# Kernel optimization log

Hardware: AMD Instinct MI355X
Metric: run time of the kernel (lower is better)

Reference implementation:

```python
import jax, jax.numpy as jnp
import numpy as np
from jax import lax

LIDAR_MAX_X = 30.0
LIDAR_MAX_Y = 30.0


def bilinear_sample(value, grid):
    """value: (bs,C,H,W); grid: (bs,nq,np,2) in [-1,1] -> (bs,C,nq,np)."""
    bs, C, H, W = value.shape
    _, nq, npts, _ = grid.shape
    gx = (grid[..., 0] + 1.0) / 2.0 * (W - 1)
    gy = (grid[..., 1] + 1.0) / 2.0 * (H - 1)
    # torch .long() truncates; in-bounds coords are non-negative so trunc == floor
    x0 = jnp.clip(gx.astype(jnp.int32), 0, W - 2)
    y0 = jnp.clip(gy.astype(jnp.int32), 0, H - 2)
    x1 = x0 + 1
    y1 = y0 + 1
    wx = jnp.clip(gx - x0.astype(gx.dtype), 0.0, 1.0).reshape(bs, 1, -1)
    wy = jnp.clip(gy - y0.astype(gy.dtype), 0.0, 1.0).reshape(bs, 1, -1)
    x0f = x0.reshape(bs, -1); x1f = x1.reshape(bs, -1)
    y0f = y0.reshape(bs, -1); y1f = y1.reshape(bs, -1)
    vflat = value.reshape(bs, C, H * W)
    gather = jax.vmap(lambda v, i: v[:, i])  # (C,HW),(N,) -> (C,N)
    v00 = gather(vflat, y0f * W + x0f)
    v01 = gather(vflat, y0f * W + x1f)
    v10 = gather(vflat, y1f * W + x0f)
    v11 = gather(vflat, y1f * W + x1f)
    sampled = (v00 * (1 - wx) * (1 - wy) + v01 * wx * (1 - wy)
               + v10 * (1 - wx) * wy + v11 * wx * wy)
    sampled = sampled.reshape(bs, C, nq, npts)
    gx0, gy0 = grid[..., 0], grid[..., 1]
    in_bounds = ((gx0 >= -1) & (gx0 <= 1) & (gy0 >= -1) & (gy0 <= 1))
    return sampled * in_bounds[:, None].astype(sampled.dtype)


def setup_inputs() -> dict:
    key = jax.random.key(0)
    ks = jax.random.split(key, 8)
    bs, nq, npts = 8, 2048, 8
    C_in, H, W = 64, 200, 200
    D = 256
    queries = jax.random.normal(ks[0], (bs, nq, D), dtype=jnp.float32)
    # lidar-frame waypoints, mostly in-bounds
    traj_points = jax.random.uniform(ks[1], (bs, nq, npts, 2), jnp.float32, -30.0, 30.0)
    bev_feature = jax.random.normal(ks[2], (bs, C_in, H, W), dtype=jnp.float32)
    attn_w = jax.random.normal(ks[3], (npts, D), dtype=jnp.float32) * 0.05
    attn_b = jnp.zeros((npts,), jnp.float32)
    out_w = jax.random.normal(ks[4], (D, D), dtype=jnp.float32) * (1.0 / np.sqrt(D))
    out_b = jnp.zeros((D,), jnp.float32)
    conv_w = jax.random.normal(ks[5], (D, C_in, 3, 3), dtype=jnp.float32) * 0.05
    conv_b = jnp.zeros((D,), jnp.float32)
    return {"queries": queries, "traj_points": traj_points, "bev_feature": bev_feature,
            "attn_w": attn_w, "attn_b": attn_b, "out_w": out_w, "out_b": out_b,
            "conv_w": conv_w, "conv_b": conv_b}


def reference(queries, traj_points, bev_feature, attn_w, attn_b, out_w, out_b, conv_w, conv_b):
    # normalize trajectory and swap (x,y) -> (y,x)
    norm = traj_points / jnp.array([LIDAR_MAX_Y, LIDAR_MAX_X], dtype=traj_points.dtype)
    grid = norm[..., ::-1]  # (bs,nq,np,2)
    # per-point attention weights
    attw = jax.nn.softmax(jnp.einsum('bqd,pd->bqp', queries, attn_w) + attn_b, axis=-1)
    # value projection: Conv3x3 + ReLU
    value = lax.conv_general_dilated(bev_feature, conv_w, (1, 1), ((1, 1), (1, 1)),
                                     dimension_numbers=('NCHW', 'OIHW', 'NCHW'))
    value = jax.nn.relu(value + conv_b[None, :, None, None])
    sampled = lax.stop_gradient(bilinear_sample(value, grid))  # (bs,C,nq,np)
    out = jnp.einsum('bcqp,bqp->bqc', sampled, attw)  # weighted sum over points
    out = jnp.einsum('bqc,dc->bqd', out, out_w) + out_b
    return out + queries  # dropout is identity in eval mode
```

## Files before the change

### kernel.cpp

```cpp
#include <hip/hip_runtime.h>

typedef unsigned short u16;
typedef _Float16 f16x8 __attribute__((ext_vector_type(8)));
typedef _Float16 f16x2 __attribute__((ext_vector_type(2)));
typedef float f32x4 __attribute__((ext_vector_type(4)));

__device__ __forceinline__ u16 f2h(float f){
  _Float16 h = (_Float16)f;
  return __builtin_bit_cast(u16, h);
}

__device__ __forceinline__ void load_lds16(const void* g, void* l){
  __builtin_amdgcn_global_load_lds((const __attribute__((address_space(1))) void*)g,
                                   (__attribute__((address_space(3))) void*)l,
                                   16, 0, 0);
}

__global__ __launch_bounds__(256) void kv9_halo(u16* __restrict__ bevT)
{
  const int i = blockIdx.x * 256 + threadIdx.x;
  if (i >= 8*804*8) return;
  const int b = i / (804*8);
  const int rem = i - b*(804*8);
  const int p = rem >> 3, c = rem & 7;
  int h, w;
  if (p < 202)      { h = 0;        w = p; }
  else if (p < 404) { h = 201;      w = p - 202; }
  else if (p < 604) { h = p - 403;  w = 0; }
  else              { h = p - 603;  w = 201; }
  const uint4 z = {0u,0u,0u,0u};
  *(uint4*)&bevT[(((size_t)b*202 + h)*202 + w)*64 + (c << 3)] = z;
}

__global__ __launch_bounds__(256) void kv9_transpose(const float* __restrict__ bev,
                                                     u16* __restrict__ bevT)
{
  __shared__ float t[64][65];
  const int tid = threadIdx.x;
  const int bid = blockIdx.x;
  const int wc = bid & 3;
  const int h  = (bid >> 2) % 200;
  const int b  = bid / 800;
  const int w0 = wc << 6;

  const int wl = (tid & 15) << 2;
  const int cb = tid >> 4;
  if (w0 + wl < 200){
    #pragma unroll
    for (int r = 0; r < 4; ++r){
      const int c = cb + (r << 4);
      const float4 v = *(const float4*)&bev[(((size_t)b*64 + c)*200 + h)*200 + (w0 + wl)];
      t[c][wl] = v.x; t[c][wl+1] = v.y; t[c][wl+2] = v.z; t[c][wl+3] = v.w;
    }
  }
  __syncthreads();
  const int c0 = (tid & 7) << 3;
  #pragma unroll
  for (int j = 0; j < 2; ++j){
    const int wl2 = (tid >> 3) + (j << 5);
    if (w0 + wl2 < 200){
      unsigned r0 = (unsigned)f2h(t[c0+0][wl2]) | ((unsigned)f2h(t[c0+1][wl2]) << 16);
      unsigned r1 = (unsigned)f2h(t[c0+2][wl2]) | ((unsigned)f2h(t[c0+3][wl2]) << 16);
      unsigned r2 = (unsigned)f2h(t[c0+4][wl2]) | ((unsigned)f2h(t[c0+5][wl2]) << 16);
      unsigned r3 = (unsigned)f2h(t[c0+6][wl2]) | ((unsigned)f2h(t[c0+7][wl2]) << 16);
      uint4 o = {r0, r1, r2, r3};
      *(uint4*)&bevT[(((size_t)b*202 + h + 1)*202 + (w0 + wl2 + 1))*64 + c0] = o;
    }
  }
}

__global__ __launch_bounds__(256) void kv9_prep(const float* __restrict__ conv_w,
                                                const float* __restrict__ out_w,
                                                u16* __restrict__ Wr,
                                                u16* __restrict__ owb)
{
  const int i = blockIdx.x * 256 + threadIdx.x;
  if (i < 9*256*64){
    const int t9 = i / (256*64);
    const int rem = i - t9*(256*64);
    const int d = rem >> 6, c = rem & 63;
    Wr[i] = f2h(conv_w[(size_t)(d*64 + c)*9 + t9]);
  } else {
    const int j = i - 9*256*64;
    if (j < 65536) owb[j] = f2h(out_w[j]);
  }
}

__global__ __launch_bounds__(256) void kv9_attw(const float* __restrict__ q,
                                                const float* __restrict__ aw,
                                                const float* __restrict__ ab,
                                                float* __restrict__ attw)
{
  const int lane = threadIdx.x & 63;
  const int bq = blockIdx.x * 4 + (threadIdx.x >> 6);
  const float4 qv = *(const float4*)&q[(size_t)bq*256 + (lane << 2)];
  float lg[8];
  #pragma unroll
  for (int p = 0; p < 8; ++p){
    const float4 wv = *(const float4*)&aw[p*256 + (lane << 2)];
    float d = qv.x*wv.x + qv.y*wv.y + qv.z*wv.z + qv.w*wv.w;
    #pragma unroll
    for (int off = 32; off > 0; off >>= 1) d += __shfl_xor(d, off);
    lg[p] = d + ab[p];
  }
  float mx = lg[0];
  #pragma unroll
  for (int p = 1; p < 8; ++p) mx = fmaxf(mx, lg[p]);
  float sum = 0.f;
  #pragma unroll
  for (int p = 0; p < 8; ++p){ lg[p] = expf(lg[p] - mx); sum += lg[p]; }
  const float inv = 1.f / sum;
  if (lane == 0){
    float4 o0 = {lg[0]*inv, lg[1]*inv, lg[2]*inv, lg[3]*inv};
    float4 o1 = {lg[4]*inv, lg[5]*inv, lg[6]*inv, lg[7]*inv};
    *(float4*)&attw[(size_t)bq*8]     = o0;
    *(float4*)&attw[(size_t)bq*8 + 4] = o1;
  }
}

__global__ __launch_bounds__(256) void kv9_conv(const u16* __restrict__ bevT,
                                                const u16* __restrict__ Wr,
                                                const float* __restrict__ conv_b,
                                                u16* __restrict__ value)
{
  __shared__ __align__(16) u16 lds[16384];
  const int tid  = threadIdx.x;
  const int bid  = (int)(blockIdx.x & 7) * 625 + (int)(blockIdx.x >> 3);
  const int n0   = (bid & 1) << 7;
  const int m0   = (bid >> 1) << 7;
  const int lane = tid & 63;
  const int wv   = tid >> 6;
  const int wm   = (wv >> 1) << 6;
  const int wn   = (wv & 1) << 6;
  const int c0   = (((tid & 7) ^ ((tid >> 3) & 7)) << 3);

  int baseA[4], baseB[4];
  #pragma unroll
  for (int i = 0; i < 4; ++i){
    const int m = m0 + (i << 5) + (tid >> 3);
    const int b = m / 40000;
    const int pix = m - b * 40000;
    const int h = pix / 200;
    const int w = pix - h * 200;
    baseA[i] = ((b*202 + h)*202 + w)*64 + c0;
    baseB[i] = (n0 + (i << 5) + (tid >> 3))*64 + c0;
  }

  const f32x4 z = {0.f, 0.f, 0.f, 0.f};
  f32x4 acc[4][4];
  #pragma unroll
  for (int mf = 0; mf < 4; ++mf)
    #pragma unroll
    for (int nf = 0; nf < 4; ++nf)
      acc[mf][nf] = z;

  const int swz = lane & 7;
  for (int t9 = 0; t9 < 9; ++t9){
    const int ky = t9 / 3;
    const int offA = (ky*202 + (t9 - ky*3))*64;
    const u16* wsrc = Wr + t9*16384;
    #pragma unroll
    for (int i = 0; i < 4; ++i){
      load_lds16(bevT + baseA[i] + offA, lds + (i << 11) + (wv << 9));
      load_lds16(wsrc + baseB[i],        lds + 8192 + (i << 11) + (wv << 9));
    }
    __syncthreads();

    f16x8 a_frag[2][4], b_frag[2][4];
    #pragma unroll
    for (int kh = 0; kh < 2; ++kh){
      const int c16 = (((kh << 2) + (lane >> 4)) ^ swz) << 3;
      #pragma unroll
      for (int f = 0; f < 4; ++f){
        a_frag[kh][f] = *(const f16x8*)&lds[(wm + (f << 4) + (lane & 15))*64 + c16];
        b_frag[kh][f] = *(const f16x8*)&lds[8192 + (wn + (f << 4) + (lane & 15))*64 + c16];
      }
    }
    #pragma unroll
    for (int kh = 0; kh < 2; ++kh)
      #pragma unroll
      for (int mf = 0; mf < 4; ++mf)
        #pragma unroll
        for (int nf = 0; nf < 4; ++nf)
          acc[mf][nf] = __builtin_amdgcn_mfma_f32_16x16x32_f16(a_frag[kh][mf], b_frag[kh][nf], acc[mf][nf], 0, 0, 0);
    __syncthreads();
  }

  #pragma unroll
  for (int nf = 0; nf < 4; ++nf){
    const int col = wn + (nf << 4) + (lane & 15);
    const float bias = conv_b[n0 + col];
    #pragma unroll
    for (int mf = 0; mf < 4; ++mf)
      #pragma unroll
      for (int rr = 0; rr < 4; ++rr){
        const int row = wm + (mf << 4) + ((lane >> 4) << 2) + rr;
        lds[row*128 + col] = f2h(fmaxf(acc[mf][nf][rr] + bias, 0.f));
      }
  }
  __syncthreads();
  #pragma unroll
  for (int it = 0; it < 8; ++it){
    const int idx = (it << 8) + tid;
    const int row = idx >> 4;
    const int ce  = (idx & 15) << 3;
    const f32x4 v = *(const f32x4*)&lds[row*128 + ce];
    *(f32x4*)&value[(size_t)(m0 + row)*256 + n0 + ce] = v;
  }
}

__global__ __launch_bounds__(256) void kv9_sample(const float* __restrict__ traj,
                                                  const float* __restrict__ attw,
                                                  const u16* __restrict__ value,
                                                  u16* __restrict__ sbh)
{
  __shared__ int   pixs[2][32];
  __shared__ float wgts[2][32];
  const int tid  = threadIdx.x;
  const int half = tid >> 7;
  const int t    = tid & 127;
  const int q    = (blockIdx.x << 1) + half;

  if (t < 8){
    const int p = t;
    const float ty = traj[((size_t)q*8 + p)*2 + 0];
    const float tx = traj[((size_t)q*8 + p)*2 + 1];
    float aw = attw[q*8 + p];
    const float gxn = tx / 30.f;
    const float gyn = ty / 30.f;
    if (!(gxn >= -1.f && gxn <= 1.f && gyn >= -1.f && gyn <= 1.f)) aw = 0.f;
    const float gx = (gxn + 1.f) * 0.5f * 199.f;
    const float gy = (gyn + 1.f) * 0.5f * 199.f;
    int x0 = (int)gx; x0 = min(max(x0, 0), 198);
    int y0 = (int)gy; y0 = min(max(y0, 0), 198);
    const float wx = fminf(fmaxf(gx - (float)x0, 0.f), 1.f);
    const float wy = fminf(fmaxf(gy - (float)y0, 0.f), 1.f);
    const int base = y0*200 + x0;
    pixs[half][p*4+0] = base;       wgts[half][p*4+0] = aw*(1.f-wx)*(1.f-wy);
    pixs[half][p*4+1] = base+1;     wgts[half][p*4+1] = aw*wx*(1.f-wy);
    pixs[half][p*4+2] = base+200;   wgts[half][p*4+2] = aw*(1.f-wx)*wy;
    pixs[half][p*4+3] = base+201;   wgts[half][p*4+3] = aw*wx*wy;
  }
  __syncthreads();
  const size_t vbase = (size_t)(q >> 11) * 40000;
  float a0 = 0.f, a1 = 0.f;
  #pragma unroll
  for (int i = 0; i < 32; ++i){
    const float w = wgts[half][i];
    const f16x2 pv = *(const f16x2*)&value[((vbase + pixs[half][i]) << 8) + (t << 1)];
    a0 = fmaf(w, (float)pv.x, a0);
    a1 = fmaf(w, (float)pv.y, a1);
  }
  const unsigned o = (unsigned)f2h(a0) | ((unsigned)f2h(a1) << 16);
  *(unsigned*)&sbh[((size_t)q << 8) + (t << 1)] = o;
}

__global__ __launch_bounds__(256) void kv9_outgemm(const u16* __restrict__ sbh,
                                                   const u16* __restrict__ owb,
                                                   const float* __restrict__ out_b,
                                                   const float* __restrict__ queries,
                                                   float* __restrict__ outp)
{
  __shared__ __align__(16) u16 lds[16384];
  const int tid  = threadIdx.x;
  const int bid  = blockIdx.x;
  const int n0   = (bid & 1) << 7;
  const int m0   = (bid >> 1) << 7;
  const int lane = tid & 63;
  const int wv   = tid >> 6;
  const int wm   = (wv >> 1) << 6;
  const int wn   = (wv & 1) << 6;
  const int c0   = (tid & 7) << 3;

  int baseA[4], baseB[4];
  #pragma unroll
  for (int i = 0; i < 4; ++i){
    baseA[i] = (m0 + (i << 5) + (tid >> 3))*256 + c0;
    baseB[i] = (n0 + (i << 5) + (tid >> 3))*256 + c0;
  }
  const f32x4 z = {0.f, 0.f, 0.f, 0.f};
  f32x4 acc[4][4];
  #pragma unroll
  for (int mf = 0; mf < 4; ++mf)
    #pragma unroll
    for (int nf = 0; nf < 4; ++nf)
      acc[mf][nf] = z;

  for (int kk = 0; kk < 4; ++kk){
    #pragma unroll
    for (int i = 0; i < 4; ++i){
      load_lds16(sbh + baseA[i] + (kk << 6), lds + (i << 11) + (wv << 9));
      load_lds16(owb + baseB[i] + (kk << 6), lds + 8192 + (i << 11) + (wv << 9));
    }
    __syncthreads();

    f16x8 a_frag[2][4], b_frag[2][4];
    #pragma unroll
    for (int kh = 0; kh < 2; ++kh){
      const int kq = (kh << 5) + ((lane >> 4) << 3);
      #pragma unroll
      for (int f = 0; f < 4; ++f){
        a_frag[kh][f] = *(const f16x8*)&lds[(wm + (f << 4) + (lane & 15))*64 + kq];
        b_frag[kh][f] = *(const f16x8*)&lds[8192 + (wn + (f << 4) + (lane & 15))*64 + kq];
      }
    }
    #pragma unroll
    for (int kh = 0; kh < 2; ++kh)
      #pragma unroll
      for (int mf = 0; mf < 4; ++mf)
        #pragma unroll
        for (int nf = 0; nf < 4; ++nf)
          acc[mf][nf] = __builtin_amdgcn_mfma_f32_16x16x32_f16(a_frag[kh][mf], b_frag[kh][nf], acc[mf][nf], 0, 0, 0);
    __syncthreads();
  }

  #pragma unroll
  for (int nf = 0; nf < 4; ++nf){
    const int col = wn + (nf << 4) + (lane & 15);
    const float ob = out_b[n0 + col];
    #pragma unroll
    for (int mf = 0; mf < 4; ++mf)
      #pragma unroll
      for (int rr = 0; rr < 4; ++rr){
        const int row = wm + (mf << 4) + ((lane >> 4) << 2) + rr;
        const size_t off = (size_t)(m0 + row)*256 + n0 + col;
        outp[off] = acc[mf][nf][rr] + ob + queries[off];
      }
  }
}

extern "C" void kernel_launch(void* const* d_in, const int* in_sizes, int n_in,
                              void* d_out, int out_size, void* d_ws, size_t ws_size,
                              hipStream_t stream)
{
  const float* queries = (const float*)d_in[0];
  const float* traj    = (const float*)d_in[1];
  const float* bev     = (const float*)d_in[2];
  const float* attn_w  = (const float*)d_in[3];
  const float* attn_b  = (const float*)d_in[4];
  const float* out_w   = (const float*)d_in[5];
  const float* out_b   = (const float*)d_in[6];
  const float* conv_w  = (const float*)d_in[7];
  const float* conv_b  = (const float*)d_in[8];
  float* outp = (float*)d_out;
  char* ws = (char*)d_ws;

  u16*   bevT  = (u16*)  (ws + 0);
  u16*   value = (u16*)  (ws + 41783296);
  u16*   Wr    = (u16*)  (ws + 205623296);
  u16*   owb   = (u16*)  (ws + 205918208);
  float* attw  = (float*)(ws + 206049280);
  u16*   sbh   = (u16*)  (ws + 206573568);

  kv9_halo     <<<201,  256, 0, stream>>>(bevT);
  kv9_transpose<<<6400, 256, 0, stream>>>(bev, bevT);
  kv9_prep     <<<832,  256, 0, stream>>>(conv_w, out_w, Wr, owb);
  kv9_attw     <<<4096, 256, 0, stream>>>(queries, attn_w, attn_b, attw);
  kv9_conv     <<<5000, 256, 0, stream>>>(bevT, Wr, conv_b, value);
  kv9_sample   <<<8192, 256, 0, stream>>>(traj, attw, value, sbh);
  kv9_outgemm  <<<256,  256, 0, stream>>>(sbh, owb, out_b, queries, outp);
}
```

Before: 206.0 us.

## Double-buffer conv LDS tiles to prefetch next tap during MFMA compute

The implicit-GEMM conv kernel now uses two LDS buffers, issuing the async global-to-LDS loads for the next 3x3 tap before computing the current one. It waits with explicit vmcnt counts and raw barriers instead of __syncthreads, and raises wave priority around the MFMA block. The aim is to hide global load latency behind matrix math. The cost is doubled LDS (64KB per block), which may lower occupancy, and hand-tuned waitcnt logic that must match the issued load count.

```diff
diff --git a/kernel.cpp b/kernel.cpp
--- a/kernel.cpp
+++ b/kernel.cpp
@@ -16,7 +16,7 @@
                                    16, 0, 0);
 }
 
-__global__ __launch_bounds__(256) void kv9_halo(u16* __restrict__ bevT)
+__global__ __launch_bounds__(256) void kv10_halo(u16* __restrict__ bevT)
 {
   const int i = blockIdx.x * 256 + threadIdx.x;
   if (i >= 8*804*8) return;
@@ -32,8 +32,8 @@
   *(uint4*)&bevT[(((size_t)b*202 + h)*202 + w)*64 + (c << 3)] = z;
 }
 
-__global__ __launch_bounds__(256) void kv9_transpose(const float* __restrict__ bev,
-                                                     u16* __restrict__ bevT)
+__global__ __launch_bounds__(256) void kv10_transpose(const float* __restrict__ bev,
+                                                      u16* __restrict__ bevT)
 {
   __shared__ float t[64][65];
   const int tid = threadIdx.x;
@@ -69,10 +69,10 @@
   }
 }
 
-__global__ __launch_bounds__(256) void kv9_prep(const float* __restrict__ conv_w,
-                                                const float* __restrict__ out_w,
-                                                u16* __restrict__ Wr,
-                                                u16* __restrict__ owb)
+__global__ __launch_bounds__(256) void kv10_prep(const float* __restrict__ conv_w,
+                                                 const float* __restrict__ out_w,
+                                                 u16* __restrict__ Wr,
+                                                 u16* __restrict__ owb)
 {
   const int i = blockIdx.x * 256 + threadIdx.x;
   if (i < 9*256*64){
@@ -86,10 +86,10 @@
   }
 }
 
-__global__ __launch_bounds__(256) void kv9_attw(const float* __restrict__ q,
-                                                const float* __restrict__ aw,
-                                                const float* __restrict__ ab,
-                                                float* __restrict__ attw)
+__global__ __launch_bounds__(256) void kv10_attw(const float* __restrict__ q,
+                                                 const float* __restrict__ aw,
+                                                 const float* __restrict__ ab,
+                                                 float* __restrict__ attw)
 {
   const int lane = threadIdx.x & 63;
   const int bq = blockIdx.x * 4 + (threadIdx.x >> 6);
@@ -118,12 +118,12 @@
   }
 }
 
-__global__ __launch_bounds__(256) void kv9_conv(const u16* __restrict__ bevT,
-                                                const u16* __restrict__ Wr,
-                                                const float* __restrict__ conv_b,
-                                                u16* __restrict__ value)
-{
-  __shared__ __align__(16) u16 lds[16384];
+__global__ __launch_bounds__(256) void kv10_conv(const u16* __restrict__ bevT,
+                                                 const u16* __restrict__ Wr,
+                                                 const float* __restrict__ conv_b,
+                                                 u16* __restrict__ value)
+{
+  __shared__ __align__(16) u16 lds[32768];
   const int tid  = threadIdx.x;
   const int bid  = (int)(blockIdx.x & 7) * 625 + (int)(blockIdx.x >> 3);
   const int n0   = (bid & 1) << 7;
@@ -154,28 +154,42 @@
     for (int nf = 0; nf < 4; ++nf)
       acc[mf][nf] = z;
 
+#define STAGE(buf, t9) do{                                                 \
+    const int ky_ = (t9)/3;                                                \
+    const int offA_ = (ky_*202 + ((t9) - ky_*3))*64;                       \
+    const u16* ws_ = Wr + (t9)*16384;                                      \
+    _Pragma("unroll")                                                      \
+    for (int i_ = 0; i_ < 4; ++i_){                                        \
+      load_lds16(bevT + baseA[i_] + offA_,                                 \
+                 lds + (buf)*16384 + (i_ << 11) + (wv << 9));              \
+      load_lds16(ws_ + baseB[i_],                                          \
+                 lds + (buf)*16384 + 8192 + (i_ << 11) + (wv << 9));       \
+    } }while(0)
+
+  STAGE(0, 0);
+
   const int swz = lane & 7;
+  #pragma unroll
   for (int t9 = 0; t9 < 9; ++t9){
-    const int ky = t9 / 3;
-    const int offA = (ky*202 + (t9 - ky*3))*64;
-    const u16* wsrc = Wr + t9*16384;
-    #pragma unroll
-    for (int i = 0; i < 4; ++i){
-      load_lds16(bevT + baseA[i] + offA, lds + (i << 11) + (wv << 9));
-      load_lds16(wsrc + baseB[i],        lds + 8192 + (i << 11) + (wv << 9));
-    }
-    __syncthreads();
-
+    const int cur = t9 & 1;
+    if (t9 < 8) STAGE(cur ^ 1, t9 + 1);
+
+    if (t9 < 8) asm volatile("s_waitcnt vmcnt(8)" ::: "memory");
+    else        asm volatile("s_waitcnt vmcnt(0)" ::: "memory");
+    __builtin_amdgcn_s_barrier();
+
+    const u16* Lb = lds + cur*16384;
     f16x8 a_frag[2][4], b_frag[2][4];
     #pragma unroll
     for (int kh = 0; kh < 2; ++kh){
       const int c16 = (((kh << 2) + (lane >> 4)) ^ swz) << 3;
       #pragma unroll
       for (int f = 0; f < 4; ++f){
-        a_frag[kh][f] = *(const f16x8*)&lds[(wm + (f << 4) + (lane & 15))*64 + c16];
-        b_frag[kh][f] = *(const f16x8*)&lds[8192 + (wn + (f << 4) + (lane & 15))*64 + c16];
+        a_frag[kh][f] = *(const f16x8*)&Lb[(wm + (f << 4) + (lane & 15))*64 + c16];
+        b_frag[kh][f] = *(const f16x8*)&Lb[8192 + (wn + (f << 4) + (lane & 15))*64 + c16];
       }
     }
+    __builtin_amdgcn_s_setprio(1);
     #pragma unroll
     for (int kh = 0; kh < 2; ++kh)
       #pragma unroll
@@ -183,8 +197,12 @@
         #pragma unroll
         for (int nf = 0; nf < 4; ++nf)
           acc[mf][nf] = __builtin_amdgcn_mfma_f32_16x16x32_f16(a_frag[kh][mf], b_frag[kh][nf], acc[mf][nf], 0, 0, 0);
-    __syncthreads();
-  }
+    __builtin_amdgcn_s_setprio(0);
+
+    asm volatile("s_waitcnt lgkmcnt(0)" ::: "memory");
+    __builtin_amdgcn_s_barrier();
+  }
+#undef STAGE
 
   #pragma unroll
   for (int nf = 0; nf < 4; ++nf){
@@ -209,10 +227,10 @@
   }
 }
 
-__global__ __launch_bounds__(256) void kv9_sample(const float* __restrict__ traj,
-                                                  const float* __restrict__ attw,
-                                                  const u16* __restrict__ value,
-                                                  u16* __restrict__ sbh)
+__global__ __launch_bounds__(256) void kv10_sample(const float* __restrict__ traj,
+                                                   const float* __restrict__ attw,
+                                                   const u16* __restrict__ value,
+                                                   u16* __restrict__ sbh)
 {
   __shared__ int   pixs[2][32];
   __shared__ float wgts[2][32];
@@ -255,11 +273,11 @@
   *(unsigned*)&sbh[((size_t)q << 8) + (t << 1)] = o;
 }
 
-__global__ __launch_bounds__(256) void kv9_outgemm(const u16* __restrict__ sbh,
-                                                   const u16* __restrict__ owb,
-                                                   const float* __restrict__ out_b,
-                                                   const float* __restrict__ queries,
-                                                   float* __restrict__ outp)
+__global__ __launch_bounds__(256) void kv10_outgemm(const u16* __restrict__ sbh,
+                                                    const u16* __restrict__ owb,
+                                                    const float* __restrict__ out_b,
+                                                    const float* __restrict__ queries,
+                                                    float* __restrict__ outp)
 {
   __shared__ __align__(16) u16 lds[16384];
   const int tid  = threadIdx.x;
@@ -352,11 +370,11 @@
   float* attw  = (float*)(ws + 206049280);
   u16*   sbh   = (u16*)  (ws + 206573568);
 
-  kv9_halo     <<<201,  256, 0, stream>>>(bevT);
-  kv9_transpose<<<6400, 256, 0, stream>>>(bev, bevT);
-  kv9_prep     <<<832,  256, 0, stream>>>(conv_w, out_w, Wr, owb);
-  kv9_attw     <<<4096, 256, 0, stream>>>(queries, attn_w, attn_b, attw);
-  kv9_conv     <<<5000, 256, 0, stream>>>(bevT, Wr, conv_b, value);
-  kv9_sample   <<<8192, 256, 0, stream>>>(traj, attw, value, sbh);
-  kv9_outgemm  <<<256,  256, 0, stream>>>(sbh, owb, out_b, queries, outp);
-}
+  kv10_halo     <<<201,  256, 0, stream>>>(bevT);
+  kv10_transpose<<<6400, 256, 0, stream>>>(bev, bevT);
+  kv10_prep     <<<832,  256, 0, stream>>>(conv_w, out_w, Wr, owb);
+  kv10_attw     <<<4096, 256, 0, stream>>>(queries, attn_w, attn_b, attw);
+  kv10_conv     <<<5000, 256, 0, stream>>>(bevT, Wr, conv_b, value);
+  kv10_sample   <<<8192, 256, 0, stream>>>(traj, attw, value, sbh);
+  kv10_outgemm  <<<256,  256, 0, stream>>>(sbh, owb, out_b, queries, outp);
+}
```

Result: no change. 202.4 us (-1.8%).

## Double-buffer conv A tiles, load B fragments to registers, remap sample blocks

Applied to the files above, without the earlier changes.

The conv kernel now double-buffers the im2col A tiles in LDS, prefetching the next tap while MFMAs run on the current one. Weight B fragments are loaded straight from global memory into registers (ping-pong bE/bO) instead of being staged through LDS. It adds manual waitcnt/barriers, setprio, and a launch-bounds occupancy hint of 2. The sample kernel's block-to-query mapping is interleaved across batches so that concurrent blocks spread over different batch slices of the value tensor. The added register pressure from B fragments and the manual vmcnt counting risk spills or ordering bugs.

```diff
diff --git a/kernel.cpp b/kernel.cpp
--- a/kernel.cpp
+++ b/kernel.cpp
@@ -16,7 +16,7 @@
                                    16, 0, 0);
 }
 
-__global__ __launch_bounds__(256) void kv9_halo(u16* __restrict__ bevT)
+__global__ __launch_bounds__(256) void kv12_halo(u16* __restrict__ bevT)
 {
   const int i = blockIdx.x * 256 + threadIdx.x;
   if (i >= 8*804*8) return;
@@ -32,8 +32,8 @@
   *(uint4*)&bevT[(((size_t)b*202 + h)*202 + w)*64 + (c << 3)] = z;
 }
 
-__global__ __launch_bounds__(256) void kv9_transpose(const float* __restrict__ bev,
-                                                     u16* __restrict__ bevT)
+__global__ __launch_bounds__(256) void kv12_transpose(const float* __restrict__ bev,
+                                                      u16* __restrict__ bevT)
 {
   __shared__ float t[64][65];
   const int tid = threadIdx.x;
@@ -69,10 +69,10 @@
   }
 }
 
-__global__ __launch_bounds__(256) void kv9_prep(const float* __restrict__ conv_w,
-                                                const float* __restrict__ out_w,
-                                                u16* __restrict__ Wr,
-                                                u16* __restrict__ owb)
+__global__ __launch_bounds__(256) void kv12_prep(const float* __restrict__ conv_w,
+                                                 const float* __restrict__ out_w,
+                                                 u16* __restrict__ Wr,
+                                                 u16* __restrict__ owb)
 {
   const int i = blockIdx.x * 256 + threadIdx.x;
   if (i < 9*256*64){
@@ -86,10 +86,10 @@
   }
 }
 
-__global__ __launch_bounds__(256) void kv9_attw(const float* __restrict__ q,
-                                                const float* __restrict__ aw,
-                                                const float* __restrict__ ab,
-                                                float* __restrict__ attw)
+__global__ __launch_bounds__(256) void kv12_attw(const float* __restrict__ q,
+                                                 const float* __restrict__ aw,
+                                                 const float* __restrict__ ab,
+                                                 float* __restrict__ attw)
 {
   const int lane = threadIdx.x & 63;
   const int bq = blockIdx.x * 4 + (threadIdx.x >> 6);
@@ -118,10 +118,10 @@
   }
 }
 
-__global__ __launch_bounds__(256) void kv9_conv(const u16* __restrict__ bevT,
-                                                const u16* __restrict__ Wr,
-                                                const float* __restrict__ conv_b,
-                                                u16* __restrict__ value)
+__global__ __launch_bounds__(256, 2) void kv12_conv(const u16* __restrict__ bevT,
+                                                    const u16* __restrict__ Wr,
+                                                    const float* __restrict__ conv_b,
+                                                    u16* __restrict__ value)
 {
   __shared__ __align__(16) u16 lds[16384];
   const int tid  = threadIdx.x;
@@ -134,7 +134,7 @@
   const int wn   = (wv & 1) << 6;
   const int c0   = (((tid & 7) ^ ((tid >> 3) & 7)) << 3);
 
-  int baseA[4], baseB[4];
+  int baseA[4];
   #pragma unroll
   for (int i = 0; i < 4; ++i){
     const int m = m0 + (i << 5) + (tid >> 3);
@@ -143,8 +143,12 @@
     const int h = pix / 200;
     const int w = pix - h * 200;
     baseA[i] = ((b*202 + h)*202 + w)*64 + c0;
-    baseB[i] = (n0 + (i << 5) + (tid >> 3))*64 + c0;
-  }
+  }
+  const int ko = (lane >> 4) << 3;
+  int rowB[4];
+  #pragma unroll
+  for (int f = 0; f < 4; ++f)
+    rowB[f] = ((n0 + wn + (f << 4) + (lane & 15)) << 6) + ko;
 
   const f32x4 z = {0.f, 0.f, 0.f, 0.f};
   f32x4 acc[4][4];
@@ -154,37 +158,79 @@
     for (int nf = 0; nf < 4; ++nf)
       acc[mf][nf] = z;
 
+  f16x8 bE[2][4], bO[2][4];
+
+#define STAGE_A(buf, t9) do{                                               \
+    const int ky_ = (t9)/3;                                                \
+    const int offA_ = (ky_*202 + ((t9) - ky_*3))*64;                       \
+    _Pragma("unroll")                                                      \
+    for (int i_ = 0; i_ < 4; ++i_)                                         \
+      load_lds16(bevT + baseA[i_] + offA_,                                 \
+                 lds + (buf)*8192 + (i_ << 11) + (wv << 9));               \
+  }while(0)
+
+#define LOADB(dst, t9) do{                                                 \
+    const u16* ws_ = Wr + (t9)*16384;                                      \
+    _Pragma("unroll")                                                      \
+    for (int f_ = 0; f_ < 4; ++f_){                                        \
+      dst[0][f_] = *(const f16x8*)&ws_[rowB[f_]];                          \
+      dst[1][f_] = *(const f16x8*)&ws_[rowB[f_] + 32];                     \
+    } }while(0)
+
   const int swz = lane & 7;
-  for (int t9 = 0; t9 < 9; ++t9){
-    const int ky = t9 / 3;
-    const int offA = (ky*202 + (t9 - ky*3))*64;
-    const u16* wsrc = Wr + t9*16384;
-    #pragma unroll
-    for (int i = 0; i < 4; ++i){
-      load_lds16(bevT + baseA[i] + offA, lds + (i << 11) + (wv << 9));
-      load_lds16(wsrc + baseB[i],        lds + 8192 + (i << 11) + (wv << 9));
-    }
-    __syncthreads();
-
-    f16x8 a_frag[2][4], b_frag[2][4];
-    #pragma unroll
-    for (int kh = 0; kh < 2; ++kh){
-      const int c16 = (((kh << 2) + (lane >> 4)) ^ swz) << 3;
-      #pragma unroll
-      for (int f = 0; f < 4; ++f){
-        a_frag[kh][f] = *(const f16x8*)&lds[(wm + (f << 4) + (lane & 15))*64 + c16];
-        b_frag[kh][f] = *(const f16x8*)&lds[8192 + (wn + (f << 4) + (lane & 15))*64 + c16];
-      }
-    }
-    #pragma unroll
-    for (int kh = 0; kh < 2; ++kh)
-      #pragma unroll
-      for (int mf = 0; mf < 4; ++mf)
-        #pragma unroll
-        for (int nf = 0; nf < 4; ++nf)
-          acc[mf][nf] = __builtin_amdgcn_mfma_f32_16x16x32_f16(a_frag[kh][mf], b_frag[kh][nf], acc[mf][nf], 0, 0, 0);
-    __syncthreads();
-  }
+
+#define TAPBODY(T, BCUR, BNXT)                                             \
+  {                                                                        \
+    if ((T) < 8){                                                          \
+      LOADB(BNXT, (T)+1);                                                  \
+      STAGE_A(((T)+1)&1, (T)+1);                                           \
+      asm volatile("s_waitcnt vmcnt(12)" ::: "memory");                    \
+    } else {                                                               \
+      asm volatile("s_waitcnt vmcnt(0)" ::: "memory");                     \
+    }                                                                      \
+    __builtin_amdgcn_s_barrier();                                          \
+    __builtin_amdgcn_sched_barrier(0);                                     \
+    const u16* Lb = lds + ((T)&1)*8192;                                    \
+    f16x8 a_frag[2][4];                                                    \
+    _Pragma("unroll")                                                      \
+    for (int kh_ = 0; kh_ < 2; ++kh_){                                     \
+      const int c16_ = (((kh_ << 2) + (lane >> 4)) ^ swz) << 3;            \
+      _Pragma("unroll")                                                    \
+      for (int f_ = 0; f_ < 4; ++f_)                                       \
+        a_frag[kh_][f_] = *(const f16x8*)&Lb[(wm + (f_ << 4) + (lane & 15))*64 + c16_]; \
+    }                                                                      \
+    __builtin_amdgcn_s_setprio(1);                                         \
+    _Pragma("unroll")                                                      \
+    for (int kh_ = 0; kh_ < 2; ++kh_)                                      \
+      _Pragma("unroll")                                                    \
+      for (int mf_ = 0; mf_ < 4; ++mf_)                                    \
+        _Pragma("unroll")                                                  \
+        for (int nf_ = 0; nf_ < 4; ++nf_)                                  \
+          acc[mf_][nf_] = __builtin_amdgcn_mfma_f32_16x16x32_f16(          \
+              a_frag[kh_][mf_], BCUR[kh_][nf_], acc[mf_][nf_], 0, 0, 0);   \
+    __builtin_amdgcn_s_setprio(0);                                         \
+    asm volatile("s_waitcnt lgkmcnt(0)" ::: "memory");                     \
+    __builtin_amdgcn_s_barrier();                                          \
+  }
+
+  LOADB(bE, 0);
+  STAGE_A(0, 0);
+
+  TAPBODY(0, bE, bO)
+  TAPBODY(1, bO, bE)
+  TAPBODY(2, bE, bO)
+  TAPBODY(3, bO, bE)
+  TAPBODY(4, bE, bO)
+  TAPBODY(5, bO, bE)
+  TAPBODY(6, bE, bO)
+  TAPBODY(7, bO, bE)
+  TAPBODY(8, bE, bO)
+
+#undef TAPBODY
+#undef LOADB
+#undef STAGE_A
+
+  __syncthreads();
 
   #pragma unroll
   for (int nf = 0; nf < 4; ++nf){
@@ -209,17 +255,18 @@
   }
 }
 
-__global__ __launch_bounds__(256) void kv9_sample(const float* __restrict__ traj,
-                                                  const float* __restrict__ attw,
-                                                  const u16* __restrict__ value,
-                                                  u16* __restrict__ sbh)
+__global__ __launch_bounds__(256) void kv12_sample(const float* __restrict__ traj,
+                                                   const float* __restrict__ attw,
+                                                   const u16* __restrict__ value,
+                                                   u16* __restrict__ sbh)
 {
   __shared__ int   pixs[2][32];
   __shared__ float wgts[2][32];
   const int tid  = threadIdx.x;
   const int half = tid >> 7;
   const int t    = tid & 127;
-  const int q    = (blockIdx.x << 1) + half;
+  const int qpair = (int)(blockIdx.x & 7) * 1024 + (int)(blockIdx.x >> 3);
+  const int q    = (qpair << 1) + half;
 
   if (t < 8){
     const int p = t;
@@ -255,11 +302,11 @@
   *(unsigned*)&sbh[((size_t)q << 8) + (t << 1)] = o;
 }
 
-__global__ __launch_bounds__(256) void kv9_outgemm(const u16* __restrict__ sbh,
-                                                   const u16* __restrict__ owb,
-                                                   const float* __restrict__ out_b,
-                                                   const float* __restrict__ queries,
-                                                   float* __restrict__ outp)
+__global__ __launch_bounds__(256) void kv12_outgemm(const u16* __restrict__ sbh,
+                                                    const u16* __restrict__ owb,
+                                                    const float* __restrict__ out_b,
+                                                    const float* __restrict__ queries,
+                                                    float* __restrict__ outp)
 {
   __shared__ __align__(16) u16 lds[16384];
   const int tid  = threadIdx.x;
@@ -352,11 +399,11 @@
   float* attw  = (float*)(ws + 206049280);
   u16*   sbh   = (u16*)  (ws + 206573568);
 
-  kv9_halo     <<<201,  256, 0, stream>>>(bevT);
-  kv9_transpose<<<6400, 256, 0, stream>>>(bev, bevT);
-  kv9_prep     <<<832,  256, 0, stream>>>(conv_w, out_w, Wr, owb);
-  kv9_attw     <<<4096, 256, 0, stream>>>(queries, attn_w, attn_b, attw);
-  kv9_conv     <<<5000, 256, 0, stream>>>(bevT, Wr, conv_b, value);
-  kv9_sample   <<<8192, 256, 0, stream>>>(traj, attw, value, sbh);
-  kv9_outgemm  <<<256,  256, 0, stream>>>(sbh, owb, out_b, queries, outp);
-}
+  kv12_halo     <<<201,  256, 0, stream>>>(bevT);
+  kv12_transpose<<<6400, 256, 0, stream>>>(bev, bevT);
+  kv12_prep     <<<832,  256, 0, stream>>>(conv_w, out_w, Wr, owb);
+  kv12_attw     <<<4096, 256, 0, stream>>>(queries, attn_w, attn_b, attw);
+  kv12_conv     <<<5000, 256, 0, stream>>>(bevT, Wr, conv_b, value);
+  kv12_sample   <<<8192, 256, 0, stream>>>(traj, attw, value, sbh);
+  kv12_outgemm  <<<256,  256, 0, stream>>>(sbh, owb, out_b, queries, outp);
+}
```

Measured after the change: 293.1 us. 1.42x slower.
